# Kernel tuning notes

Measured on AMD Instinct MI355X. Metric: run time of the kernel, lower is better.

Reference implementation:

```python
import jax, jax.numpy as jnp
import numpy as np

B, L, H, KV, D, HID = 2, 2048, 16, 4, 128, 2048
EPS = 1e-6
ROPE_BASE = 10000.0


def _rotate_half(x):
    x1, x2 = jnp.split(x, 2, axis=-1)
    return jnp.concatenate((-x2, x1), axis=-1)


def _rms_norm(x, w):
    xf = x.astype(jnp.float32)
    var = jnp.mean(xf * xf, axis=-1, keepdims=True)
    return w * (xf * jax.lax.rsqrt(var + EPS)).astype(x.dtype)


def setup_inputs() -> dict:
    key = jax.random.key(0)
    ks = jax.random.split(key, 6)
    hidden_states = jax.random.normal(ks[0], (B, L, HID), dtype=jnp.float32)
    # rotary embeddings (standard rope table)
    inv_freq = 1.0 / (ROPE_BASE ** (jnp.arange(0, D, 2, dtype=jnp.float32) / D))
    pos = jnp.arange(L, dtype=jnp.float32)
    freqs = pos[:, None] * inv_freq[None, :]          # [L, D/2]
    emb = jnp.concatenate((freqs, freqs), axis=-1)    # [L, D]
    cos = jnp.broadcast_to(jnp.cos(emb)[None], (B, L, D))
    sin = jnp.broadcast_to(jnp.sin(emb)[None], (B, L, D))
    s = 0.02
    Wq = jax.random.normal(ks[1], (HID, H * D), dtype=jnp.float32) * s
    Wk = jax.random.normal(ks[2], (HID, KV * D), dtype=jnp.float32) * s
    Wv = jax.random.normal(ks[3], (HID, KV * D), dtype=jnp.float32) * s
    Wo = jax.random.normal(ks[4], (H * D, HID), dtype=jnp.float32) * s
    q_norm_w = jnp.ones((D,), dtype=jnp.float32)
    k_norm_w = jnp.ones((D,), dtype=jnp.float32)
    return {"hidden_states": hidden_states, "cos": cos, "sin": sin,
            "Wq": Wq, "Wk": Wk, "Wv": Wv, "Wo": Wo,
            "q_norm_w": q_norm_w, "k_norm_w": k_norm_w}


def reference(hidden_states, cos, sin, Wq, Wk, Wv, Wo, q_norm_w, k_norm_w):
    scale = D ** -0.5
    n_rep = H // KV
    q = (hidden_states @ Wq).reshape(B, L, H, D)
    k = (hidden_states @ Wk).reshape(B, L, KV, D)
    v = (hidden_states @ Wv).reshape(B, L, KV, D)
    q = _rms_norm(q, q_norm_w).transpose(0, 2, 1, 3)   # [B,H,L,D]
    k = _rms_norm(k, k_norm_w).transpose(0, 2, 1, 3)   # [B,KV,L,D]
    v = v.transpose(0, 2, 1, 3)                         # [B,KV,L,D]
    c = cos[:, None]                                    # [B,1,L,D]
    s = sin[:, None]
    q = q * c + _rotate_half(q) * s
    k = k * c + _rotate_half(k) * s
    # GQA without materializing repeated K/V: group query heads per kv head.
    qg = q.reshape(B, KV, n_rep, L, D)
    scores = jnp.einsum('bgrld,bgmd->bgrlm', qg, k) * scale
    attn = jax.nn.softmax(scores, axis=-1)
    out = jnp.einsum('bgrlm,bgmd->bgrld', attn, v)      # [B,KV,n_rep,L,D]
    out = out.reshape(B, H, L, D).transpose(0, 2, 1, 3).reshape(B, L, H * D)
    return out @ Wo
```

## Files before the change

kernel.cpp:

```cpp
#include <hip/hip_runtime.h>

typedef unsigned short u16;
typedef unsigned int u32;
typedef short bf16x8 __attribute__((ext_vector_type(8)));
typedef float f32x4 __attribute__((ext_vector_type(4)));

#define B_ 2
#define L_ 2048
#define H_ 16
#define KV_ 4
#define D_ 128
#define HID_ 2048

#define QSCALE (0.08838834764831845f * 1.4426950408889634f)

__device__ __forceinline__ u16 f2bf(float f) {
  union { float f; u32 u; } v; v.f = f;
  u32 u = v.u;
  return (u16)((u + 0x7FFFu + ((u >> 16) & 1u)) >> 16);
}
__device__ __forceinline__ float bf2f(u16 h) {
  union { u32 u; float f; } v; v.u = ((u32)h) << 16;
  return v.f;
}
__device__ __forceinline__ u32 pkbf(float a, float b) {
  union { float f; u32 u; } x, y; x.f = a; y.f = b;
  return ((x.u + 0x8000u) >> 16) | ((y.u + 0x8000u) & 0xffff0000u);
}
__device__ __forceinline__ void gl_lds16(const void* g, void* l) {
  __builtin_amdgcn_global_load_lds((__attribute__((address_space(1))) void*)(g),
                                   (__attribute__((address_space(3))) void*)(l),
                                   16, 0, 0);
}

__global__ void k_prep(const float* __restrict__ hidden, u16* __restrict__ Xb,
                       const float* __restrict__ Wq, const float* __restrict__ Wk,
                       const float* __restrict__ Wv, const float* __restrict__ Wo,
                       u16* __restrict__ Wtqkv, u16* __restrict__ Wto) {
  __shared__ float t[32][33];
  int id = blockIdx.x;
  if (id < 8192) {
    int i = id * 256 + threadIdx.x;
    float4 v = ((const float4*)hidden)[i];
    u32 a = (u32)f2bf(v.x) | ((u32)f2bf(v.y) << 16);
    u32 b = (u32)f2bf(v.z) | ((u32)f2bf(v.w) << 16);
    ((uint2*)Xb)[i] = make_uint2(a, b);
    return;
  }
  id -= 8192;
  const float* src; u16* dst; int C; int ct, rt;
  if (id < 4096)      { src = Wq; dst = Wtqkv;               C = 2048; ct = id & 63; rt = id >> 6; }
  else if (id < 5120) { id -= 4096; src = Wk; dst = Wtqkv + 2048 * 2048; C = 512; ct = id & 15; rt = id >> 4; }
  else if (id < 6144) { id -= 5120; src = Wv; dst = Wtqkv + 2560 * 2048; C = 512; ct = id & 15; rt = id >> 4; }
  else                { id -= 6144; src = Wo; dst = Wto;     C = 2048; ct = id & 63; rt = id >> 6; }
  const int R = 2048;
  int c0 = ct * 32, r0 = rt * 32;
  int tx = threadIdx.x & 31, ty = threadIdx.x >> 5;
  for (int i = ty; i < 32; i += 8)
    t[i][tx] = src[(size_t)(r0 + i) * C + c0 + tx];
  __syncthreads();
  for (int i = ty; i < 32; i += 8)
    dst[(size_t)(c0 + i) * R + r0 + tx] = f2bf(t[tx][i]);
}

__global__ __launch_bounds__(256, 3) void k_gemm_qkv(
    const u16* __restrict__ A, const u16* __restrict__ Bt,
    const float* __restrict__ cosp, const float* __restrict__ sinp,
    const float* __restrict__ qw, const float* __restrict__ kw,
    u16* __restrict__ Qb, u16* __restrict__ Kb, u16* __restrict__ Vtb) {
  __shared__ u16 smem[24576];
  u16* As = smem;
  u16* Bs = smem + 8192;
  const int tid = threadIdx.x;
  const int wave = tid >> 6, lane = tid & 63;
  const int wr = wave >> 1, wc = wave & 1;
  const int quad = lane >> 4, fm = lane & 15;
  const int K = 2048;
  const int m0 = blockIdx.y * 128, n0 = blockIdx.x * 128;
  f32x4 acc[4][4];
  for (int i = 0; i < 4; ++i)
    for (int j = 0; j < 4; ++j)
      for (int r = 0; r < 4; ++r) acc[i][j][r] = 0.0f;

  const int lrow = lane >> 3;
  const int lcol = (lane & 7) * 8;
  const int fk = quad * 8;

  for (int kt = 0; kt < K; kt += 64) {
    for (int p = 0; p < 4; ++p) {
      int roff = wave * 32 + p * 8 + lrow;
      gl_lds16(A + (size_t)(m0 + roff) * K + kt + lcol,
               As + wave * 2048 + p * 512 + lane * 8);
      gl_lds16(Bt + (size_t)(n0 + roff) * K + kt + lcol,
               Bs + wave * 2048 + p * 512 + lane * 8);
    }
    __syncthreads();
    for (int s = 0; s < 2; ++s) {
      bf16x8 af[4], bfr[4];
      for (int i = 0; i < 4; ++i)
        af[i] = *(const bf16x8*)(As + (wr * 64 + i * 16 + fm) * 64 + s * 32 + fk);
      for (int j = 0; j < 4; ++j)
        bfr[j] = *(const bf16x8*)(Bs + (wc * 64 + j * 16 + fm) * 64 + s * 32 + fk);
      for (int i = 0; i < 4; ++i)
        for (int j = 0; j < 4; ++j)
          acc[i][j] = __builtin_amdgcn_mfma_f32_16x16x32_bf16(af[i], bfr[j],
                                                              acc[i][j], 0, 0, 0);
    }
    __syncthreads();
  }

  u16* Cs = smem;
  for (int i = 0; i < 4; ++i)
    for (int j = 0; j < 4; ++j)
      for (int r = 0; r < 4; ++r)
        Cs[(wr * 64 + i * 16 + quad * 4 + r) * 136 + wc * 64 + j * 16 + fm] =
            f2bf(acc[i][j][r]);
  __syncthreads();

  const int head = blockIdx.x;
  const int b = m0 >> 11, l0 = m0 & 2047;
  if (head < 20) {
    const int isq = head < 16;
    const float* wv = isq ? qw : kw;
    const int half = lane >> 5, sl = lane & 31;
    u16* outp = isq ? (Qb + (size_t)(b * H_ + head) * L_ * D_)
                    : (Kb + (size_t)(b * KV_ + head - 16) * L_ * D_);
    const float4 wvv = *(const float4*)(wv + sl * 4);
    for (int it = 0; it < 16; ++it) {
      int r = wave * 32 + it * 2 + half;
      const u16* crow = Cs + r * 136 + sl * 4;
      u32 c01 = *(const u32*)crow;
      u32 c23 = *(const u32*)(crow + 2);
      float x0 = bf2f((u16)(c01 & 0xffff)), x1 = bf2f((u16)(c01 >> 16));
      float x2 = bf2f((u16)(c23 & 0xffff)), x3 = bf2f((u16)(c23 >> 16));
      float ssq = (x0 * x0 + x1 * x1) + (x2 * x2 + x3 * x3);
      ssq += __shfl_xor(ssq, 1);
      ssq += __shfl_xor(ssq, 2);
      ssq += __shfl_xor(ssq, 4);
      ssq += __shfl_xor(ssq, 8);
      ssq += __shfl_xor(ssq, 16);
      float rr = rsqrtf(ssq * (1.0f / 128.0f) + 1e-6f);
      float n0 = x0 * rr * wvv.x, n1 = x1 * rr * wvv.y;
      float n2 = x2 * rr * wvv.z, n3 = x3 * rr * wvv.w;
      float p0 = __shfl_xor(n0, 16), p1 = __shfl_xor(n1, 16);
      float p2 = __shfl_xor(n2, 16), p3 = __shfl_xor(n3, 16);
      float sgn = (sl < 16) ? -1.0f : 1.0f;
      int tok = m0 + r;
      const float4 cv = *(const float4*)(cosp + (size_t)tok * 128 + sl * 4);
      const float4 sv = *(const float4*)(sinp + (size_t)tok * 128 + sl * 4);
      float o0 = n0 * cv.x + sgn * p0 * sv.x;
      float o1 = n1 * cv.y + sgn * p1 * sv.y;
      float o2 = n2 * cv.z + sgn * p2 * sv.z;
      float o3 = n3 * cv.w + sgn * p3 * sv.w;
      if (isq) { o0 *= QSCALE; o1 *= QSCALE; o2 *= QSCALE; o3 *= QSCALE; }
      u32 lo = (u32)f2bf(o0) | ((u32)f2bf(o1) << 16);
      u32 hi = (u32)f2bf(o2) | ((u32)f2bf(o3) << 16);
      *(uint2*)(outp + (size_t)(l0 + r) * D_ + sl * 4) = make_uint2(lo, hi);
    }
  } else {
    int g = head - 20;
    int d = tid >> 1, lh = tid & 1;
    u16* dst = Vtb + ((size_t)(b * KV_ + g) * D_ + d) * L_ + l0 + lh * 64;
    for (int a2 = 0; a2 < 2; ++a2)
      for (int bc = 0; bc < 8; ++bc) {
        int b2 = bc & 1, c = bc >> 1;
        int ls = lh * 64 + a2 * 32 + 16 * b2 + 4 * c;
        u32 lo = (u32)Cs[ls * 136 + d] | ((u32)Cs[(ls + 1) * 136 + d] << 16);
        u32 hi = (u32)Cs[(ls + 2) * 136 + d] | ((u32)Cs[(ls + 3) * 136 + d] << 16);
        *(uint2*)(dst + a2 * 32 + 8 * c + 4 * b2) = make_uint2(lo, hi);
      }
  }
}

template <int OUT_BF16>
__global__ __launch_bounds__(256, 3) void k_gemm_bt(
    const u16* __restrict__ A, const u16* __restrict__ Bt, void* __restrict__ Cv,
    int M, int N, int K) {
  __shared__ u16 smem[16384];
  u16* As = smem;
  u16* Bs = smem + 8192;
  const int tid = threadIdx.x;
  const int wave = tid >> 6, lane = tid & 63;
  const int wr = wave >> 1, wc = wave & 1;
  const int quad = lane >> 4, fm = lane & 15;
  const int m0 = blockIdx.y * 128, n0 = blockIdx.x * 128;
  f32x4 acc[4][4];
  for (int i = 0; i < 4; ++i)
    for (int j = 0; j < 4; ++j)
      for (int r = 0; r < 4; ++r) acc[i][j][r] = 0.0f;

  const int lrow = lane >> 3;
  const int lcol = (lane & 7) * 8;
  const int fk = quad * 8;

  for (int kt = 0; kt < K; kt += 64) {
    for (int p = 0; p < 4; ++p) {
      int roff = wave * 32 + p * 8 + lrow;
      gl_lds16(A + (size_t)(m0 + roff) * K + kt + lcol,
               As + wave * 2048 + p * 512 + lane * 8);
      gl_lds16(Bt + (size_t)(n0 + roff) * K + kt + lcol,
               Bs + wave * 2048 + p * 512 + lane * 8);
    }
    __syncthreads();
    for (int s = 0; s < 2; ++s) {
      bf16x8 af[4], bfr[4];
      for (int i = 0; i < 4; ++i)
        af[i] = *(const bf16x8*)(As + (wr * 64 + i * 16 + fm) * 64 + s * 32 + fk);
      for (int j = 0; j < 4; ++j)
        bfr[j] = *(const bf16x8*)(Bs + (wc * 64 + j * 16 + fm) * 64 + s * 32 + fk);
      for (int i = 0; i < 4; ++i)
        for (int j = 0; j < 4; ++j)
          acc[i][j] = __builtin_amdgcn_mfma_f32_16x16x32_bf16(af[i], bfr[j],
                                                              acc[i][j], 0, 0, 0);
    }
    __syncthreads();
  }

  if (OUT_BF16) {
    u16* Cs = smem;
    for (int hh = 0; hh < 2; ++hh) {
      if (hh) __syncthreads();
      if (wr == hh)
        for (int i = 0; i < 4; ++i)
          for (int j = 0; j < 4; ++j)
            for (int r = 0; r < 4; ++r)
              Cs[(i * 16 + quad * 4 + r) * 136 + wc * 64 + j * 16 + fm] =
                  f2bf(acc[i][j][r]);
      __syncthreads();
      for (int it = 0; it < 4; ++it) {
        int row = it * 16 + (tid >> 4);
        int col = (tid & 15) * 8;
        uint4 v = *(const uint4*)(Cs + row * 136 + col);
        *(uint4*)((u16*)Cv + (size_t)(m0 + hh * 64 + row) * N + n0 + col) = v;
      }
    }
  } else {
    float* Cf = (float*)smem;
    for (int p = 0; p < 4; ++p) {
      if (p) __syncthreads();
      if (wr == (p >> 1))
        for (int ii = 0; ii < 2; ++ii) {
          int i = 2 * (p & 1) + ii;
          for (int j = 0; j < 4; ++j)
            for (int r = 0; r < 4; ++r)
              Cf[(ii * 16 + quad * 4 + r) * 132 + wc * 64 + j * 16 + fm] =
                  acc[i][j][r];
        }
      __syncthreads();
      for (int it = 0; it < 4; ++it) {
        int row = it * 8 + (tid >> 5);
        int col = (tid & 31) * 4;
        float4 v = *(const float4*)(Cf + row * 132 + col);
        *(float4*)((float*)Cv + (size_t)(m0 + p * 32 + row) * N + n0 + col) = v;
      }
    }
  }
}

__global__ __launch_bounds__(256, 2) void k_attn(const u16* __restrict__ Qb,
                                                 const u16* __restrict__ Kb,
                                                 const u16* __restrict__ Vtb,
                                                 u16* __restrict__ AO) {
  __shared__ u16 smem[32768];
  const int tid = threadIdx.x, wave = tid >> 6, lane = tid & 63;
  const int quad = lane >> 4, fm = lane & 15;
  const int f7 = fm & 7;
  const int bid = blockIdx.x;
  const int xcd = bid & 7, w = bid >> 3;
  const int b = xcd >> 2, g = xcd & 3;
  const int h = g * 4 + (w & 3);
  const int qt = w >> 2;
  const int bh = b * 16 + h;
  const u16* Kg = Kb + ((size_t)(b * KV_ + g)) * L_ * D_;
  const u16* Vg = Vtb + ((size_t)(b * KV_ + g)) * D_ * L_;

  const u16* Qg = Qb + ((size_t)bh * L_ + qt * 128 + wave * 32 + fm) * D_;
  bf16x8 qf1[4], qf2[4];
  for (int ks = 0; ks < 4; ++ks) {
    qf1[ks] = *(const bf16x8*)(Qg + ks * 32 + quad * 8);
    qf2[ks] = *(const bf16x8*)(Qg + 16 * D_ + ks * 32 + quad * 8);
  }

  f32x4 o1[8], o2[8];
  for (int f = 0; f < 8; ++f)
    for (int r = 0; r < 4; ++r) { o1[f][r] = 0.0f; o2[f][r] = 0.0f; }
  float lr1 = 0.0f, lr2 = 0.0f;
  const f32x4 fz = {0.0f, 0.0f, 0.0f, 0.0f};

  const int eK = wave * 2048 + (lane << 3);
  const int cK = lane & 15;
  const int cV = lane & 7;

#define STAGE(kt_, buf_)                                                      \
  {                                                                           \
    u16* Kd = smem + (buf_)*16384;                                            \
    u16* Vd = smem + (buf_)*16384 + 8192;                                     \
    for (int p = 0; p < 4; ++p) {                                             \
      int e = eK + p * 512;                                                   \
      int rowK = e >> 7;                                                      \
      int gK = (cK & 8) | ((cK & 7) ^ (rowK & 7));                            \
      gl_lds16(Kg + (size_t)((kt_)*64 + rowK) * 128 + gK * 8, Kd + e);        \
      int rowV = e >> 6;                                                      \
      int gV = cV ^ (rowV & 7);                                               \
      gl_lds16(Vg + (size_t)rowV * L_ + (kt_)*64 + gV * 8, Vd + e);           \
    }                                                                         \
  }

  STAGE(0, 0);
  for (int kt = 0; kt < 32; ++kt) {
    __syncthreads();
    if (kt + 1 < 32) STAGE(kt + 1, (kt + 1) & 1);
    const u16* Ks = smem + (kt & 1) * 16384;
    const u16* Vs = Ks + 8192;

    f32x4 s1[4], s2[4];
    __builtin_amdgcn_s_setprio(1);
    {
      int cp = (quad & 8) | (quad ^ f7);
      for (int n = 0; n < 4; ++n) {
        bf16x8 kf = *(const bf16x8*)(Ks + (n * 16 + fm) * 128 + cp * 8);
        s1[n] = __builtin_amdgcn_mfma_f32_16x16x32_bf16(kf, qf1[0], fz, 0, 0, 0);
        s2[n] = __builtin_amdgcn_mfma_f32_16x16x32_bf16(kf, qf2[0], fz, 0, 0, 0);
      }
    }
    for (int ks = 1; ks < 4; ++ks) {
      int c = 4 * ks + quad;
      int cp = (c & 8) | ((c & 7) ^ f7);
      for (int n = 0; n < 4; ++n) {
        bf16x8 kf = *(const bf16x8*)(Ks + (n * 16 + fm) * 128 + cp * 8);
        s1[n] = __builtin_amdgcn_mfma_f32_16x16x32_bf16(kf, qf1[ks], s1[n], 0, 0, 0);
        s2[n] = __builtin_amdgcn_mfma_f32_16x16x32_bf16(kf, qf2[ks], s2[n], 0, 0, 0);
      }
    }
    __builtin_amdgcn_s_setprio(0);

    u32 pk1[4][2], pk2[4][2];
    float rs1 = 0.0f, rs2 = 0.0f;
    for (int n = 0; n < 4; ++n) {
      float a0 = __builtin_amdgcn_exp2f(s1[n][0]);
      float a1 = __builtin_amdgcn_exp2f(s1[n][1]);
      float a2 = __builtin_amdgcn_exp2f(s1[n][2]);
      float a3 = __builtin_amdgcn_exp2f(s1[n][3]);
      rs1 += (a0 + a1) + (a2 + a3);
      pk1[n][0] = pkbf(a0, a1);
      pk1[n][1] = pkbf(a2, a3);
      float b0 = __builtin_amdgcn_exp2f(s2[n][0]);
      float b1 = __builtin_amdgcn_exp2f(s2[n][1]);
      float b2 = __builtin_amdgcn_exp2f(s2[n][2]);
      float b3 = __builtin_amdgcn_exp2f(s2[n][3]);
      rs2 += (b0 + b1) + (b2 + b3);
      pk2[n][0] = pkbf(b0, b1);
      pk2[n][1] = pkbf(b2, b3);
    }
    lr1 += rs1;
    lr2 += rs2;

    __builtin_amdgcn_s_setprio(1);
    for (int ks2 = 0; ks2 < 2; ++ks2) {
      union { u32 u[4]; bf16x8 v; } pa1, pa2;
      pa1.u[0] = pk1[2 * ks2][0];
      pa1.u[1] = pk1[2 * ks2][1];
      pa1.u[2] = pk1[2 * ks2 + 1][0];
      pa1.u[3] = pk1[2 * ks2 + 1][1];
      pa2.u[0] = pk2[2 * ks2][0];
      pa2.u[1] = pk2[2 * ks2][1];
      pa2.u[2] = pk2[2 * ks2 + 1][0];
      pa2.u[3] = pk2[2 * ks2 + 1][1];
      int chunk = (4 * ks2 + quad) ^ f7;
      for (int f = 0; f < 8; ++f) {
        bf16x8 vv = *(const bf16x8*)(Vs + (f * 16 + fm) * 64 + chunk * 8);
        o1[f] = __builtin_amdgcn_mfma_f32_16x16x32_bf16(pa1.v, vv, o1[f], 0, 0, 0);
        o2[f] = __builtin_amdgcn_mfma_f32_16x16x32_bf16(pa2.v, vv, o2[f], 0, 0, 0);
      }
    }
    __builtin_amdgcn_s_setprio(0);
  }
#undef STAGE

  const size_t tok0 = (size_t)b * L_ + qt * 128;
  for (int grp = 0; grp < 2; ++grp) {
    f32x4* o = grp ? o2 : o1;
    float lr = grp ? lr2 : lr1;
    lr += __shfl_xor(lr, 16);
    lr += __shfl_xor(lr, 32);
    float li = 1.0f / lr;
    float l0 = __shfl(li, (lane & 48) | (quad * 4 + 0));
    float l1 = __shfl(li, (lane & 48) | (quad * 4 + 1));
    float l2 = __shfl(li, (lane & 48) | (quad * 4 + 2));
    float l3 = __shfl(li, (lane & 48) | (quad * 4 + 3));
    __syncthreads();
    for (int f = 0; f < 8; ++f) {
      int e = (wave * 16 + quad * 4) * 136 + f * 16 + fm;
      smem[e] = f2bf(o[f][0] * l0);
      smem[e + 136] = f2bf(o[f][1] * l1);
      smem[e + 272] = f2bf(o[f][2] * l2);
      smem[e + 408] = f2bf(o[f][3] * l3);
    }
    __syncthreads();
    for (int it = 0; it < 8; ++it) {
      int crow = (tid >> 6) * 16 + it * 2 + (lane >> 5);
      int q = (crow >> 4) * 32 + grp * 16 + (crow & 15);
      int cc = (lane & 31) * 4;
      uint2 v = *(const uint2*)(smem + crow * 136 + cc);
      *(uint2*)(AO + (tok0 + q) * (H_ * D_) + h * D_ + cc) = v;
    }
  }
}

extern "C" void kernel_launch(void* const* d_in, const int* in_sizes, int n_in,
                              void* d_out, int out_size, void* d_ws,
                              size_t ws_size, hipStream_t stream) {
  const float* hidden = (const float*)d_in[0];
  const float* cosp = (const float*)d_in[1];
  const float* sinp = (const float*)d_in[2];
  const float* Wq = (const float*)d_in[3];
  const float* Wk = (const float*)d_in[4];
  const float* Wv = (const float*)d_in[5];
  const float* Wo = (const float*)d_in[6];
  const float* qw = (const float*)d_in[7];
  const float* kw = (const float*)d_in[8];
  float* out = (float*)d_out;

  char* w = (char*)d_ws;
  u16* Xb = (u16*)(w);
  u16* Wtqkv = (u16*)(w + (16u << 20));
  u16* Wto = (u16*)(w + (28u << 20));
  u16* Qb = (u16*)(w + (36u << 20));
  u16* Kb = (u16*)(w + (52u << 20));
  u16* Vtb = (u16*)(w + (56u << 20));
  u16* AO = Xb;

  k_prep<<<18432, 256, 0, stream>>>(hidden, Xb, Wq, Wk, Wv, Wo, Wtqkv, Wto);
  k_gemm_qkv<<<dim3(24, 32), 256, 0, stream>>>(Xb, Wtqkv, cosp, sinp, qw, kw,
                                               Qb, Kb, Vtb);
  k_attn<<<dim3(512), 256, 0, stream>>>(Qb, Kb, Vtb, AO);
  k_gemm_bt<0><<<dim3(16, 32), 256, 0, stream>>>(AO, Wto, out, 4096, 2048, 2048);
}
```

Measured before the change: 318.6 us.

## Rewrite QKV GEMM as 256x256 tile, 8-wave, double-buffered pipelined kernel

Replaces the 128x128 single-buffered QKV GEMM with a 256x256 tile processed by 512 threads. It uses 128KB dynamic LDS for double buffering, XOR-swizzled LDS layout, interleaved global-to-LDS staging between MFMA quarters with explicit vmcnt waits and barriers, and a grouped block-index swizzle for L2 reuse. The epilogue is reworked to process four 128x128 quadrants sequentially through LDS for the RMSNorm/RoPE and V-transpose stores. The aim is to cut global traffic per FLOP and hide load latency. The cost is a grid of only 192 blocks with heavy LDS use and low occupancy.

After: 305.4 us. 4.1% less time.

```diff
diff --git a/kernel.cpp b/kernel.cpp
--- a/kernel.cpp
+++ b/kernel.cpp
@@ -32,6 +32,17 @@
                                    (__attribute__((address_space(3))) void*)(l),
                                    16, 0, 0);
 }
+
+template <int N> __device__ __forceinline__ void vmwait() {
+  asm volatile("s_waitcnt vmcnt(%0)" ::"n"(N) : "memory");
+}
+#define BARRIER()                                                         \
+  do {                                                                    \
+    asm volatile("" ::: "memory");                                        \
+    __builtin_amdgcn_s_barrier();                                         \
+    asm volatile("" ::: "memory");                                        \
+    __builtin_amdgcn_sched_barrier(0);                                    \
+  } while (0)
 
 __global__ void k_prep(const float* __restrict__ hidden, u16* __restrict__ Xb,
                        const float* __restrict__ Wq, const float* __restrict__ Wk,
@@ -63,19 +74,197 @@
     dst[(size_t)(c0 + i) * R + r0 + tx] = f2bf(t[tx][i]);
 }
 
-__global__ __launch_bounds__(256, 3) void k_gemm_qkv(
+__global__ __launch_bounds__(512, 2) void k_gemm_qkv(
     const u16* __restrict__ A, const u16* __restrict__ Bt,
     const float* __restrict__ cosp, const float* __restrict__ sinp,
     const float* __restrict__ qw, const float* __restrict__ kw,
     u16* __restrict__ Qb, u16* __restrict__ Kb, u16* __restrict__ Vtb) {
-  __shared__ u16 smem[24576];
-  u16* As = smem;
-  u16* Bs = smem + 8192;
+  extern __shared__ char smem[];
+  const int tid = threadIdx.x;
+  const int wave = tid >> 6, lane = tid & 63;
+  const int wm = wave >> 2, wn = wave & 3;
+  const int quad = lane >> 4, fm = lane & 15;
+  const int f7 = fm & 7;
+
+  const int bid = blockIdx.x;
+  const int swz = (bid & 7) * 24 + (bid >> 3);
+  const int by = swz / 12, bx = swz % 12;
+  const int m0 = by * 256, n0 = bx * 256;
+
+  const u16* Ag = A + (size_t)m0 * 2048;
+  const u16* Bg = Bt + (size_t)n0 * 2048;
+  const int schunk = (lane & 7) ^ ((lane >> 3) & 7);
+
+  f32x4 acc[8][4];
+#pragma unroll
+  for (int i = 0; i < 8; ++i)
+#pragma unroll
+    for (int j = 0; j < 4; ++j)
+#pragma unroll
+      for (int r = 0; r < 4; ++r) acc[i][j][r] = 0.0f;
+
+  bf16x8 af[4][2], bf[4][2];
+  const int ArowB = (wm * 128 + fm) * 128;
+  const int BrowB = (wn * 64 + fm) * 128;
+  const int kc[2] = {(quad ^ f7) * 16, ((quad ^ 4) ^ f7) * 16};
+
+#define STAGE_A(qa_, kk_, bb_)                                               \
+  _Pragma("unroll") for (int q = 0; q < 2; ++q) {                            \
+    int ldsoff = (bb_)*32768 + q * 16384 + (qa_)*8192 + wave * 1024 + lane * 16; \
+    int grow = q * 128 + (qa_)*64 + wave * 8 + (lane >> 3);                  \
+    gl_lds16(Ag + (size_t)grow * 2048 + (kk_)*64 + schunk * 8, smem + ldsoff); \
+  }
+#define STAGE_B(qb_, kk_, bb_)                                               \
+  _Pragma("unroll") for (int q = 0; q < 2; ++q) {                            \
+    int gg = q * 2 + (wave >> 2);                                            \
+    int ldsoff = 65536 + (bb_)*32768 + gg * 8192 + (qb_)*4096 +              \
+                 (wave & 3) * 1024 + lane * 16;                              \
+    int grow = gg * 64 + (qb_)*32 + (wave & 3) * 8 + (lane >> 3);            \
+    gl_lds16(Bg + (size_t)grow * 2048 + (kk_)*64 + schunk * 8, smem + ldsoff); \
+  }
+#define LDA4(bb_, roff_)                                                     \
+  _Pragma("unroll") for (int i = 0; i < 4; ++i)                              \
+    _Pragma("unroll") for (int ks = 0; ks < 2; ++ks)                         \
+      af[i][ks] = *(const bf16x8*)(smem + (bb_)*32768 + ArowB + (roff_) +    \
+                                   i * 2048 + kc[ks]);
+#define LDB2(bb_, j0_)                                                       \
+  _Pragma("unroll") for (int j = 0; j < 2; ++j)                              \
+    _Pragma("unroll") for (int ks = 0; ks < 2; ++ks)                         \
+      bf[(j0_) + j][ks] = *(const bf16x8*)(smem + 65536 + (bb_)*32768 +      \
+                                           BrowB + ((j0_) + j) * 2048 + kc[ks]);
+#define MFMA_Q(I0_, J0_)                                                     \
+  __builtin_amdgcn_s_setprio(1);                                             \
+  _Pragma("unroll") for (int i = 0; i < 4; ++i)                              \
+    _Pragma("unroll") for (int j = 0; j < 2; ++j)                            \
+      _Pragma("unroll") for (int ks = 0; ks < 2; ++ks)                       \
+        acc[(I0_) + i][(J0_) + j] = __builtin_amdgcn_mfma_f32_16x16x32_bf16( \
+            af[i][ks], bf[(J0_) + j][ks], acc[(I0_) + i][(J0_) + j], 0, 0, 0); \
+  __builtin_amdgcn_s_setprio(0);
+#define TILE(kt_, bb_, ST_, W0_, W1_, W2_)                                   \
+  {                                                                          \
+    vmwait<W0_>(); BARRIER();                                                \
+    LDA4(bb_, 0); LDB2(bb_, 0);                                              \
+    if (ST_) { STAGE_A(0, (kt_) + 1, (bb_) ^ 1); }                           \
+    MFMA_Q(0, 0);                                                            \
+    vmwait<W1_>(); BARRIER();                                                \
+    LDB2(bb_, 2);                                                            \
+    if (ST_) { STAGE_B(0, (kt_) + 1, (bb_) ^ 1); }                           \
+    MFMA_Q(0, 2);                                                            \
+    vmwait<W2_>(); BARRIER();                                                \
+    LDA4(bb_, 8192);                                                         \
+    if (ST_) { STAGE_B(1, (kt_) + 1, (bb_) ^ 1); }                           \
+    MFMA_Q(4, 0);                                                            \
+    if (ST_) { STAGE_A(1, (kt_) + 1, (bb_) ^ 1); }                           \
+    MFMA_Q(4, 2);                                                            \
+  }
+
+  STAGE_A(0, 0, 0);
+  STAGE_B(0, 0, 0);
+  STAGE_B(1, 0, 0);
+  STAGE_A(1, 0, 0);
+
+#pragma unroll 1
+  for (int t2 = 0; t2 < 30; t2 += 2) {
+    TILE(t2, 0, 1, 4, 4, 4);
+    TILE(t2 + 1, 1, 1, 4, 4, 4);
+  }
+  TILE(30, 0, 1, 4, 4, 4);
+  TILE(31, 1, 0, 4, 2, 0);
+
+#undef TILE
+#undef MFMA_Q
+#undef LDB2
+#undef LDA4
+#undef STAGE_B
+#undef STAGE_A
+
+  u16* Cs = (u16*)smem;
+  const int head2 = bx * 2;
+  const int bL = by >> 3;
+  const int l0 = m0 & 2047;
+  __syncthreads();
+#pragma unroll 1
+  for (int qq = 0; qq < 4; ++qq) {
+    const int qm = qq >> 1, qn = qq & 1;
+    __syncthreads();
+    if (wm == qm && (wn >> 1) == qn) {
+#pragma unroll
+      for (int i = 0; i < 8; ++i)
+#pragma unroll
+        for (int j = 0; j < 4; ++j)
+#pragma unroll
+          for (int r = 0; r < 4; ++r)
+            Cs[(i * 16 + quad * 4 + r) * 136 + (wn & 1) * 64 + j * 16 + fm] =
+                f2bf(acc[i][j][r]);
+    }
+    __syncthreads();
+    const int hq = head2 + qn;
+    const int tok0 = m0 + qm * 128;
+    const int l0q = l0 + qm * 128;
+    if (hq < 20) {
+      const int isq = hq < 16;
+      const float* wv = isq ? qw : kw;
+      const int half = lane >> 5, sl = lane & 31;
+      u16* outp = isq ? (Qb + (size_t)(bL * H_ + hq) * L_ * D_)
+                      : (Kb + (size_t)(bL * KV_ + hq - 16) * L_ * D_);
+      const float4 wvv = *(const float4*)(wv + sl * 4);
+      for (int it = 0; it < 8; ++it) {
+        int r = wave * 16 + it * 2 + half;
+        const u16* crow = Cs + r * 136 + sl * 4;
+        u32 c01 = *(const u32*)crow;
+        u32 c23 = *(const u32*)(crow + 2);
+        float x0 = bf2f((u16)(c01 & 0xffff)), x1 = bf2f((u16)(c01 >> 16));
+        float x2 = bf2f((u16)(c23 & 0xffff)), x3 = bf2f((u16)(c23 >> 16));
+        float ssq = (x0 * x0 + x1 * x1) + (x2 * x2 + x3 * x3);
+        ssq += __shfl_xor(ssq, 1);
+        ssq += __shfl_xor(ssq, 2);
+        ssq += __shfl_xor(ssq, 4);
+        ssq += __shfl_xor(ssq, 8);
+        ssq += __shfl_xor(ssq, 16);
+        float rr = rsqrtf(ssq * (1.0f / 128.0f) + 1e-6f);
+        float nn0 = x0 * rr * wvv.x, nn1 = x1 * rr * wvv.y;
+        float nn2 = x2 * rr * wvv.z, nn3 = x3 * rr * wvv.w;
+        float p0 = __shfl_xor(nn0, 16), p1 = __shfl_xor(nn1, 16);
+        float p2 = __shfl_xor(nn2, 16), p3 = __shfl_xor(nn3, 16);
+        float sgn = (sl < 16) ? -1.0f : 1.0f;
+        int tok = tok0 + r;
+        const float4 cv = *(const float4*)(cosp + (size_t)tok * 128 + sl * 4);
+        const float4 sv = *(const float4*)(sinp + (size_t)tok * 128 + sl * 4);
+        float o0 = nn0 * cv.x + sgn * p0 * sv.x;
+        float o1 = nn1 * cv.y + sgn * p1 * sv.y;
+        float o2 = nn2 * cv.z + sgn * p2 * sv.z;
+        float o3 = nn3 * cv.w + sgn * p3 * sv.w;
+        if (isq) { o0 *= QSCALE; o1 *= QSCALE; o2 *= QSCALE; o3 *= QSCALE; }
+        u32 lo = (u32)f2bf(o0) | ((u32)f2bf(o1) << 16);
+        u32 hi = (u32)f2bf(o2) | ((u32)f2bf(o3) << 16);
+        *(uint2*)(outp + (size_t)(l0q + r) * D_ + sl * 4) = make_uint2(lo, hi);
+      }
+    } else {
+      int g = hq - 20;
+      int d = tid >> 2, a2 = (tid >> 1) & 1, lh = tid & 1;
+      u16* dst = Vtb + ((size_t)(bL * KV_ + g) * D_ + d) * L_ + l0q + lh * 64;
+      for (int bc = 0; bc < 8; ++bc) {
+        int b2 = bc & 1, c = bc >> 1;
+        int ls = lh * 64 + a2 * 32 + 16 * b2 + 4 * c;
+        u32 lo = (u32)Cs[ls * 136 + d] | ((u32)Cs[(ls + 1) * 136 + d] << 16);
+        u32 hi = (u32)Cs[(ls + 2) * 136 + d] | ((u32)Cs[(ls + 3) * 136 + d] << 16);
+        *(uint2*)(dst + a2 * 32 + 8 * c + 4 * b2) = make_uint2(lo, hi);
+      }
+    }
+  }
+}
+
+template <int OUT_BF16>
+__global__ __launch_bounds__(256, 3) void k_gemm_bt(
+    const u16* __restrict__ A, const u16* __restrict__ Bt, void* __restrict__ Cv,
+    int M, int N, int K) {
+  __shared__ u16 smem2[16384];
+  u16* As = smem2;
+  u16* Bs = smem2 + 8192;
   const int tid = threadIdx.x;
   const int wave = tid >> 6, lane = tid & 63;
   const int wr = wave >> 1, wc = wave & 1;
   const int quad = lane >> 4, fm = lane & 15;
-  const int K = 2048;
   const int m0 = blockIdx.y * 128, n0 = blockIdx.x * 128;
   f32x4 acc[4][4];
   for (int i = 0; i < 4; ++i)
@@ -109,115 +298,8 @@
     __syncthreads();
   }
 
-  u16* Cs = smem;
-  for (int i = 0; i < 4; ++i)
-    for (int j = 0; j < 4; ++j)
-      for (int r = 0; r < 4; ++r)
-        Cs[(wr * 64 + i * 16 + quad * 4 + r) * 136 + wc * 64 + j * 16 + fm] =
-            f2bf(acc[i][j][r]);
-  __syncthreads();
-
-  const int head = blockIdx.x;
-  const int b = m0 >> 11, l0 = m0 & 2047;
-  if (head < 20) {
-    const int isq = head < 16;
-    const float* wv = isq ? qw : kw;
-    const int half = lane >> 5, sl = lane & 31;
-    u16* outp = isq ? (Qb + (size_t)(b * H_ + head) * L_ * D_)
-                    : (Kb + (size_t)(b * KV_ + head - 16) * L_ * D_);
-    const float4 wvv = *(const float4*)(wv + sl * 4);
-    for (int it = 0; it < 16; ++it) {
-      int r = wave * 32 + it * 2 + half;
-      const u16* crow = Cs + r * 136 + sl * 4;
-      u32 c01 = *(const u32*)crow;
-      u32 c23 = *(const u32*)(crow + 2);
-      float x0 = bf2f((u16)(c01 & 0xffff)), x1 = bf2f((u16)(c01 >> 16));
-      float x2 = bf2f((u16)(c23 & 0xffff)), x3 = bf2f((u16)(c23 >> 16));
-      float ssq = (x0 * x0 + x1 * x1) + (x2 * x2 + x3 * x3);
-      ssq += __shfl_xor(ssq, 1);
-      ssq += __shfl_xor(ssq, 2);
-      ssq += __shfl_xor(ssq, 4);
-      ssq += __shfl_xor(ssq, 8);
-      ssq += __shfl_xor(ssq, 16);
-      float rr = rsqrtf(ssq * (1.0f / 128.0f) + 1e-6f);
-      float n0 = x0 * rr * wvv.x, n1 = x1 * rr * wvv.y;
-      float n2 = x2 * rr * wvv.z, n3 = x3 * rr * wvv.w;
-      float p0 = __shfl_xor(n0, 16), p1 = __shfl_xor(n1, 16);
-      float p2 = __shfl_xor(n2, 16), p3 = __shfl_xor(n3, 16);
-      float sgn = (sl < 16) ? -1.0f : 1.0f;
-      int tok = m0 + r;
-      const float4 cv = *(const float4*)(cosp + (size_t)tok * 128 + sl * 4);
-      const float4 sv = *(const float4*)(sinp + (size_t)tok * 128 + sl * 4);
-      float o0 = n0 * cv.x + sgn * p0 * sv.x;
-      float o1 = n1 * cv.y + sgn * p1 * sv.y;
-      float o2 = n2 * cv.z + sgn * p2 * sv.z;
-      float o3 = n3 * cv.w + sgn * p3 * sv.w;
-      if (isq) { o0 *= QSCALE; o1 *= QSCALE; o2 *= QSCALE; o3 *= QSCALE; }
-      u32 lo = (u32)f2bf(o0) | ((u32)f2bf(o1) << 16);
-      u32 hi = (u32)f2bf(o2) | ((u32)f2bf(o3) << 16);
-      *(uint2*)(outp + (size_t)(l0 + r) * D_ + sl * 4) = make_uint2(lo, hi);
-    }
-  } else {
-    int g = head - 20;
-    int d = tid >> 1, lh = tid & 1;
-    u16* dst = Vtb + ((size_t)(b * KV_ + g) * D_ + d) * L_ + l0 + lh * 64;
-    for (int a2 = 0; a2 < 2; ++a2)
-      for (int bc = 0; bc < 8; ++bc) {
-        int b2 = bc & 1, c = bc >> 1;
-        int ls = lh * 64 + a2 * 32 + 16 * b2 + 4 * c;
-        u32 lo = (u32)Cs[ls * 136 + d] | ((u32)Cs[(ls + 1) * 136 + d] << 16);
-        u32 hi = (u32)Cs[(ls + 2) * 136 + d] | ((u32)Cs[(ls + 3) * 136 + d] << 16);
-        *(uint2*)(dst + a2 * 32 + 8 * c + 4 * b2) = make_uint2(lo, hi);
-      }
-  }
-}
-
-template <int OUT_BF16>
-__global__ __launch_bounds__(256, 3) void k_gemm_bt(
-    const u16* __restrict__ A, const u16* __restrict__ Bt, void* __restrict__ Cv,
-    int M, int N, int K) {
-  __shared__ u16 smem[16384];
-  u16* As = smem;
-  u16* Bs = smem + 8192;
-  const int tid = threadIdx.x;
-  const int wave = tid >> 6, lane = tid & 63;
-  const int wr = wave >> 1, wc = wave & 1;
-  const int quad = lane >> 4, fm = lane & 15;
-  const int m0 = blockIdx.y * 128, n0 = blockIdx.x * 128;
-  f32x4 acc[4][4];
-  for (int i = 0; i < 4; ++i)
-    for (int j = 0; j < 4; ++j)
-      for (int r = 0; r < 4; ++r) acc[i][j][r] = 0.0f;
-
-  const int lrow = lane >> 3;
-  const int lcol = (lane & 7) * 8;
-  const int fk = quad * 8;
-
-  for (int kt = 0; kt < K; kt += 64) {
-    for (int p = 0; p < 4; ++p) {
-      int roff = wave * 32 + p * 8 + lrow;
-      gl_lds16(A + (size_t)(m0 + roff) * K + kt + lcol,
-               As + wave * 2048 + p * 512 + lane * 8);
-      gl_lds16(Bt + (size_t)(n0 + roff) * K + kt + lcol,
-               Bs + wave * 2048 + p * 512 + lane * 8);
-    }
-    __syncthreads();
-    for (int s = 0; s < 2; ++s) {
-      bf16x8 af[4], bfr[4];
-      for (int i = 0; i < 4; ++i)
-        af[i] = *(const bf16x8*)(As + (wr * 64 + i * 16 + fm) * 64 + s * 32 + fk);
-      for (int j = 0; j < 4; ++j)
-        bfr[j] = *(const bf16x8*)(Bs + (wc * 64 + j * 16 + fm) * 64 + s * 32 + fk);
-      for (int i = 0; i < 4; ++i)
-        for (int j = 0; j < 4; ++j)
-          acc[i][j] = __builtin_amdgcn_mfma_f32_16x16x32_bf16(af[i], bfr[j],
-                                                              acc[i][j], 0, 0, 0);
-    }
-    __syncthreads();
-  }
-
   if (OUT_BF16) {
-    u16* Cs = smem;
+    u16* Cs = smem2;
     for (int hh = 0; hh < 2; ++hh) {
       if (hh) __syncthreads();
       if (wr == hh)
@@ -235,7 +317,7 @@
       }
     }
   } else {
-    float* Cf = (float*)smem;
+    float* Cf = (float*)smem2;
     for (int p = 0; p < 4; ++p) {
       if (p) __syncthreads();
       if (wr == (p >> 1))
@@ -261,7 +343,7 @@
                                                  const u16* __restrict__ Kb,
                                                  const u16* __restrict__ Vtb,
                                                  u16* __restrict__ AO) {
-  __shared__ u16 smem[32768];
+  __shared__ u16 smem3[32768];
   const int tid = threadIdx.x, wave = tid >> 6, lane = tid & 63;
   const int quad = lane >> 4, fm = lane & 15;
   const int f7 = fm & 7;
@@ -293,8 +375,8 @@
 
 #define STAGE(kt_, buf_)                                                      \
   {                                                                           \
-    u16* Kd = smem + (buf_)*16384;                                            \
-    u16* Vd = smem + (buf_)*16384 + 8192;                                     \
+    u16* Kd = smem3 + (buf_)*16384;                                           \
+    u16* Vd = smem3 + (buf_)*16384 + 8192;                                    \
     for (int p = 0; p < 4; ++p) {                                             \
       int e = eK + p * 512;                                                   \
       int rowK = e >> 7;                                                      \
@@ -310,7 +392,7 @@
   for (int kt = 0; kt < 32; ++kt) {
     __syncthreads();
     if (kt + 1 < 32) STAGE(kt + 1, (kt + 1) & 1);
-    const u16* Ks = smem + (kt & 1) * 16384;
+    const u16* Ks = smem3 + (kt & 1) * 16384;
     const u16* Vs = Ks + 8192;
 
     f32x4 s1[4], s2[4];
@@ -391,17 +473,17 @@
     __syncthreads();
     for (int f = 0; f < 8; ++f) {
       int e = (wave * 16 + quad * 4) * 136 + f * 16 + fm;
-      smem[e] = f2bf(o[f][0] * l0);
-      smem[e + 136] = f2bf(o[f][1] * l1);
-      smem[e + 272] = f2bf(o[f][2] * l2);
-      smem[e + 408] = f2bf(o[f][3] * l3);
+      smem3[e] = f2bf(o[f][0] * l0);
+      smem3[e + 136] = f2bf(o[f][1] * l1);
+      smem3[e + 272] = f2bf(o[f][2] * l2);
+      smem3[e + 408] = f2bf(o[f][3] * l3);
     }
     __syncthreads();
     for (int it = 0; it < 8; ++it) {
       int crow = (tid >> 6) * 16 + it * 2 + (lane >> 5);
       int q = (crow >> 4) * 32 + grp * 16 + (crow & 15);
       int cc = (lane & 31) * 4;
-      uint2 v = *(const uint2*)(smem + crow * 136 + cc);
+      uint2 v = *(const uint2*)(smem3 + crow * 136 + cc);
       *(uint2*)(AO + (tok0 + q) * (H_ * D_) + h * D_ + cc) = v;
     }
   }
@@ -431,8 +513,8 @@
   u16* AO = Xb;
 
   k_prep<<<18432, 256, 0, stream>>>(hidden, Xb, Wq, Wk, Wv, Wo, Wtqkv, Wto);
-  k_gemm_qkv<<<dim3(24, 32), 256, 0, stream>>>(Xb, Wtqkv, cosp, sinp, qw, kw,
-                                               Qb, Kb, Vtb);
+  k_gemm_qkv<<<dim3(192), dim3(512), 131072, stream>>>(Xb, Wtqkv, cosp, sinp,
+                                                       qw, kw, Qb, Kb, Vtb);
   k_attn<<<dim3(512), 256, 0, stream>>>(Qb, Kb, Vtb, AO);
   k_gemm_bt<0><<<dim3(16, 32), 256, 0, stream>>>(AO, Wto, out, 4096, 2048, 2048);
 }
```
